# Optimization experiments

Measured on AMD Instinct MI355X. Metric: run time of the kernel, lower is better.

## Reference

```python
import jax, jax.numpy as jnp
import numpy as np

OBS_DIM, ACT_DIM, H_DIM = 128, 32, 512
B, T, N = 32, 64, 64


def setup_inputs() -> dict:
    key = jax.random.key(0)
    ks = jax.random.split(key, 8)
    in_dim = OBS_DIM + ACT_DIM
    s_ih = 1.0 / np.sqrt(H_DIM)
    return {
        "obs_hist": jax.random.normal(ks[0], (B, T, N, OBS_DIM), jnp.float32),
        "action_hist": jax.random.normal(ks[1], (B, T, N, ACT_DIM), jnp.float32),
        "w_ih": jax.random.uniform(ks[2], (3 * H_DIM, in_dim), jnp.float32, -s_ih, s_ih),
        "w_hh": jax.random.uniform(ks[3], (3 * H_DIM, H_DIM), jnp.float32, -s_ih, s_ih),
        "b_ih": jax.random.uniform(ks[4], (3 * H_DIM,), jnp.float32, -s_ih, s_ih),
        "b_hh": jax.random.uniform(ks[5], (3 * H_DIM,), jnp.float32, -s_ih, s_ih),
        "w_dec": jax.random.uniform(ks[6], (OBS_DIM, H_DIM), jnp.float32, -s_ih, s_ih),
        "b_dec": jax.random.uniform(ks[7], (OBS_DIM,), jnp.float32, -s_ih, s_ih),
        "horizon": 63,
    }


def _gru_cell(x, h, w_ih, w_hh, b_ih, b_hh):
    # torch.nn.GRUCell gate order: r, z, n
    gi = x @ w_ih.T + b_ih          # (bn, 3h)
    gh = h @ w_hh.T + b_hh          # (bn, 3h)
    i_r, i_z, i_n = jnp.split(gi, 3, axis=-1)
    h_r, h_z, h_n = jnp.split(gh, 3, axis=-1)
    r = jax.nn.sigmoid(i_r + h_r)
    z = jax.nn.sigmoid(i_z + h_z)
    n = jnp.tanh(i_n + r * h_n)
    return (1.0 - z) * n + z * h


def reference(obs_hist, action_hist, w_ih, w_hh, b_ih, b_hh, w_dec, b_dec, horizon):
    b, t, n, d = obs_hist.shape
    hd = w_hh.shape[1]
    # teacher forcing with horizon <= t-1: step s consumes obs_hist[:, s]
    # time-leading inputs for scan: (horizon, b*n, d+a)
    xs = jnp.concatenate([obs_hist[:, :horizon], action_hist[:, :horizon]], axis=-1)
    xs = xs.transpose(1, 0, 2, 3).reshape(horizon, b * n, -1)
    h0 = jnp.zeros((b * n, hd), obs_hist.dtype)

    def step(h, inp):
        h = _gru_cell(inp, h, w_ih, w_hh, b_ih, b_hh)
        pred = h @ w_dec.T + b_dec  # (bn, d)
        return h, (pred, h)

    _, (preds, hs) = jax.lax.scan(step, h0, xs)
    preds = preds.reshape(horizon, b, n, d).transpose(1, 0, 2, 3)  # (b, horizon, n, d)
    hs = hs.reshape(horizon, b, n, hd).transpose(1, 0, 2, 3)       # (b, horizon, n, h)
    return preds, hs
```

## Files before the change

kernel.cpp:

```cpp
#include <hip/hip_runtime.h>
#include <stdint.h>

typedef _Float16 half_t;
typedef _Float16 half8 __attribute__((ext_vector_type(8)));
typedef _Float16 half4 __attribute__((ext_vector_type(4)));
typedef float f32x16 __attribute__((ext_vector_type(16)));
typedef float f32x4  __attribute__((ext_vector_type(4)));

#define OBS_D 128
#define ACT_D 32
#define IN_D  160
#define H_D   512
#define T_H   63
#define NROWS 2048
#define KTOT  672
#define KT_ALL 42
#define KT_X   10
#define KT_H   32
#define NT_ALL 48
#define NBLK   64
#define NG     16
#define NC     16
#define NFLAG_WORDS (NG*T_H*NC)
#define PRED_ELEMS (NROWS*T_H*OBS_D)

#define ZERO16 {0.f,0.f,0.f,0.f,0.f,0.f,0.f,0.f,0.f,0.f,0.f,0.f,0.f,0.f,0.f,0.f}
#define MFMA16 __builtin_amdgcn_mfma_f32_32x32x16_f16

__device__ __forceinline__ float sigm(float x) {
    return __builtin_amdgcn_rcpf(1.0f + __expf(-x));
}
__device__ __forceinline__ float tanh_f(float x) {
    return 2.0f * __builtin_amdgcn_rcpf(1.0f + __expf(-2.0f * x)) - 1.0f;
}

__global__ void pack_w(const float* __restrict__ w_ih, const float* __restrict__ w_hh,
                       const float* __restrict__ w_dec,
                       half_t* __restrict__ wpack, half_t* __restrict__ wdpack) {
    int idx = blockIdx.x * 256 + threadIdx.x;
    int lane = idx & 63;
    int m = lane & 31;
    int khalf = lane >> 5;
    if (idx < NT_ALL * KT_ALL * 64) {
        int kt = (idx >> 6) % KT_ALL;
        int nt = idx / (64 * KT_ALL);
        int n = nt * 32 + m;
        int k0 = kt * 16 + khalf * 8;
        half8 o;
        #pragma unroll
        for (int j = 0; j < 8; ++j) {
            int k = k0 + j;
            float v = (k < IN_D) ? w_ih[(size_t)n * IN_D + k]
                                 : w_hh[(size_t)n * H_D + (k - IN_D)];
            o[j] = (half_t)v;
        }
        *(half8*)(wpack + (size_t)idx * 8) = o;
    } else {
        int r = idx - NT_ALL * KT_ALL * 64;
        int kt = (r >> 6) % 32;
        int nt = r / (64 * 32);
        int n = nt * 32 + m;
        int k0 = kt * 16 + khalf * 8;
        half8 o;
        #pragma unroll
        for (int j = 0; j < 8; ++j) o[j] = (half_t)w_dec[(size_t)n * H_D + k0 + j];
        *(half8*)(wdpack + (size_t)r * 8) = o;
    }
}

__global__ void pack_x(const float* __restrict__ obs, const float* __restrict__ act,
                       half_t* __restrict__ xfrag, unsigned* __restrict__ flags) {
    int idx = blockIdx.x * 256 + threadIdx.x;
    if (idx < NFLAG_WORDS)
        __hip_atomic_store(&flags[idx], 0u, __ATOMIC_RELAXED, __HIP_MEMORY_SCOPE_AGENT);
    int lane = idx & 63;
    int kt = (idx >> 6) % KT_X;
    int t  = (idx / (64 * KT_X)) % T_H;
    int rb = idx / (64 * KT_X * T_H);
    int m = lane & 31;
    int row = rb * 32 + m;
    int b = row >> 6, nn = row & 63;
    int k0 = kt * 16 + (lane >> 5) * 8;
    const float* ob = obs + (((size_t)(b * 64 + t)) * 64 + nn) * OBS_D;
    const float* ac = act + (((size_t)(b * 64 + t)) * 64 + nn) * ACT_D;
    half8 o;
    #pragma unroll
    for (int j = 0; j < 8; ++j) {
        int k = k0 + j;
        float v = (k < OBS_D) ? ob[k] : ac[k - OBS_D];
        o[j] = (half_t)v;
    }
    *(half8*)(xfrag + (size_t)idx * 8) = o;
}

__global__ __launch_bounds__(256, 1) void gru_main(
        const half_t* __restrict__ wpack, const half_t* __restrict__ xfrag,
        const float* __restrict__ b_ih, const float* __restrict__ b_hh,
        float* __restrict__ out, unsigned* __restrict__ flags) {
    __shared__ __align__(16) half_t Bl[3 * KT_ALL * 512];

    const int tid = threadIdx.x;
    const int wv = tid >> 6;
    const int lane = tid & 63;
    const int col = lane & 31;
    const int khalf = lane >> 5;
    const int mbase = khalf * 4;
    const int g  = blockIdx.x & 15;
    const int cb = blockIdx.x >> 4;

    {
        uint4* dst = (uint4*)Bl;
        #pragma unroll
        for (int gi = 0; gi < 3; ++gi) {
            const uint4* src = (const uint4*)(wpack +
                ((size_t)(gi * 16 + cb) * KT_ALL) * 512);
            for (int s = tid; s < KT_ALL * 64; s += 256)
                dst[gi * (KT_ALL * 64) + s] = src[s];
        }
    }

    const int d = cb * 32 + col;
    const float br = b_ih[d] + b_hh[d];
    const float bz = b_ih[512 + d] + b_hh[512 + d];
    const float bi = b_ih[1024 + d];
    const float bh = b_hh[1024 + d];

    const int bq  = g * 2 + (wv >> 1);
    const int nnq = (wv & 1) * 32;
    const int rrow = lane & 31;

    const half_t* xb = xfrag + ((size_t)(g * 4 + wv) * T_H) * (KT_X * 512) + lane * 8;

    float* hsw = out + (size_t)PRED_ELEMS
               + ((size_t)bq * T_H) * (64 * 512) + (size_t)nnq * 512;

    float h[16];
    #pragma unroll
    for (int i = 0; i < 16; ++i) h[i] = 0.0f;

    const half8* Br = (const half8*)Bl;
    const half8* Bz = (const half8*)(Bl + 21504);
    const half8* Bn = (const half8*)(Bl + 43008);

    __syncthreads();

    for (int t = 0; ; ++t) {
        f32x16 ar, az, ai, ah;
        #pragma unroll
        for (int i = 0; i < 16; ++i) { ar[i] = br; az[i] = bz; ai[i] = bi; ah[i] = bh; }

        {
            const half_t* xt = xb + (size_t)t * (KT_X * 512);
            #pragma unroll
            for (int kt = 0; kt < KT_X; ++kt) {
                half8 a = *(const half8*)(xt + kt * 512);
                ar = MFMA16(a, Br[kt * 64 + lane], ar, 0, 0, 0);
                az = MFMA16(a, Bz[kt * 64 + lane], az, 0, 0, 0);
                ai = MFMA16(a, Bn[kt * 64 + lane], ai, 0, 0, 0);
            }
        }
        if (t > 0) {
            const float* hp = hsw + (size_t)(t - 1) * (64 * 512)
                            + (size_t)rrow * 512 + khalf * 8;
            #pragma unroll 8
            for (int kt = KT_X; kt < KT_ALL; ++kt) {
                int hd = (kt - KT_X) * 16;
                f32x4 v0 = *(const f32x4*)(hp + hd);
                f32x4 v1 = *(const f32x4*)(hp + hd + 4);
                half8 a;
                a[0] = (half_t)v0[0]; a[1] = (half_t)v0[1];
                a[2] = (half_t)v0[2]; a[3] = (half_t)v0[3];
                a[4] = (half_t)v1[0]; a[5] = (half_t)v1[1];
                a[6] = (half_t)v1[2]; a[7] = (half_t)v1[3];
                ar = MFMA16(a, Br[kt * 64 + lane], ar, 0, 0, 0);
                az = MFMA16(a, Bz[kt * 64 + lane], az, 0, 0, 0);
                ah = MFMA16(a, Bn[kt * 64 + lane], ah, 0, 0, 0);
            }
        }

        {
            float* hw = hsw + (size_t)t * (64 * 512);
            #pragma unroll
            for (int r = 0; r < 16; ++r) {
                int m = (r & 3) + 8 * (r >> 2) + mbase;
                float rr = sigm(ar[r]);
                float zz2 = sigm(az[r]);
                float nn2 = tanh_f(ai[r] + rr * ah[r]);
                float hv = (1.0f - zz2) * nn2 + zz2 * h[r];
                h[r] = hv;
                __hip_atomic_store(hw + (size_t)m * 512 + d, hv,
                                   __ATOMIC_RELAXED, __HIP_MEMORY_SCOPE_AGENT);
            }
        }

        if (t == T_H - 1) break;

        __syncthreads();

        unsigned* fb = flags + (size_t)(g * T_H + t) * NC;
        if (tid == 0)
            __hip_atomic_store(fb + cb, 1u,
                               __ATOMIC_RELEASE, __HIP_MEMORY_SCOPE_AGENT);
        if (tid < NC) {
            int guard = 0;
            while (__hip_atomic_load(fb + tid, __ATOMIC_ACQUIRE,
                                     __HIP_MEMORY_SCOPE_AGENT) == 0u) {
                if (++guard > (1 << 15)) break;
            }
        }
        __syncthreads();
    }
}

#define DPAD 520
__global__ __launch_bounds__(256) void dec_k(
        const float* __restrict__ hs, const half_t* __restrict__ wdpack,
        const float* __restrict__ b_dec, float* __restrict__ preds) {
    __shared__ __align__(16) half_t Ab[32 * DPAD];
    const int tid = threadIdx.x, w = tid >> 6, lane = tid & 63;
    const size_t row0 = (size_t)blockIdx.x * 32;

    const float* src = hs + row0 * 512;
    #pragma unroll
    for (int c = 0; c < 16; ++c) {
        int f = c * 1024 + tid * 4;
        f32x4 v = *(const f32x4*)(src + f);
        int m = f >> 9, colc = f & 511;
        half4 o;
        o[0] = (half_t)v[0]; o[1] = (half_t)v[1]; o[2] = (half_t)v[2]; o[3] = (half_t)v[3];
        *(half4*)(Ab + m * DPAD + colc) = o;
    }
    __syncthreads();

    f32x16 acc = ZERO16;
    const half_t* wd = wdpack + ((size_t)w * 32) * 512 + lane * 8;
    const int mA = lane & 31, k0 = (lane >> 5) * 8;
    #pragma unroll 4
    for (int kt = 0; kt < 32; ++kt) {
        half8 a = *(const half8*)(Ab + mA * DPAD + kt * 16 + k0);
        half8 b = *(const half8*)(wd + kt * 512);
        acc = MFMA16(a, b, acc, 0, 0, 0);
    }
    const int colD = w * 32 + (lane & 31);
    const float bd = b_dec[colD];
    #pragma unroll
    for (int r = 0; r < 16; ++r) {
        int m = (r & 3) + 8 * (r >> 2) + 4 * (lane >> 5);
        preds[(row0 + m) * 128 + colD] = acc[r] + bd;
    }
}

extern "C" void kernel_launch(void* const* d_in, const int* in_sizes, int n_in,
                              void* d_out, int out_size, void* d_ws, size_t ws_size,
                              hipStream_t stream) {
    const float* obs   = (const float*)d_in[0];
    const float* act   = (const float*)d_in[1];
    const float* w_ih  = (const float*)d_in[2];
    const float* w_hh  = (const float*)d_in[3];
    const float* b_ih  = (const float*)d_in[4];
    const float* b_hh  = (const float*)d_in[5];
    const float* w_dec = (const float*)d_in[6];
    const float* b_dec = (const float*)d_in[7];
    float* out = (float*)d_out;

    half_t* wpack  = (half_t*)d_ws;
    half_t* wdpack = wpack + (size_t)NT_ALL * KT_ALL * 512;
    half_t* xfrag  = wdpack + (size_t)4 * 32 * 512;
    unsigned* flags = (unsigned*)(xfrag + (size_t)NBLK * T_H * (KT_X * 512));

    hipLaunchKernelGGL(pack_w, dim3(536), dim3(256), 0, stream,
                       w_ih, w_hh, w_dec, wpack, wdpack);
    hipLaunchKernelGGL(pack_x, dim3(10080), dim3(256), 0, stream,
                       obs, act, xfrag, flags);
    hipLaunchKernelGGL(gru_main, dim3(NG * NC), dim3(256), 0, stream,
                       wpack, xfrag, b_ih, b_hh, out, flags);
    hipLaunchKernelGGL(dec_k, dim3(NROWS * T_H / 32), dim3(256), 0, stream,
                       out + (size_t)PRED_ELEMS, wdpack, b_dec, out);
}
```

Baseline: 1.505 ms.

## Overlap next-step input projection with grid barrier wait and prefetch h loads

Computes the x-part MFMA accumulation for step t+1 between signalling the flag and spinning on the cross-block barrier, so input-projection work hides the synchronisation latency. It also software-pipelines the fp32 h-state loads in the recurrent part, issuing the next 8 loads ahead of the MFMAs. The flag store and load are relaxed from release/acquire to relaxed, which removes fences but risks other blocks reading stale h values. The spin guard limit is doubled.

```diff
diff --git a/kernel.cpp b/kernel.cpp
--- a/kernel.cpp
+++ b/kernel.cpp
@@ -142,39 +142,56 @@
     const half8* Bz = (const half8*)(Bl + 21504);
     const half8* Bn = (const half8*)(Bl + 43008);
 
+    f32x16 ar, az, ai, ah;
+
+#define ACC_INIT() do { _Pragma("unroll") \
+    for (int i_ = 0; i_ < 16; ++i_) { ar[i_]=br; az[i_]=bz; ai[i_]=bi; ah[i_]=bh; } \
+    } while (0)
+
+#define XPART(TT) do { const half_t* xt_ = xb + (size_t)(TT) * (KT_X * 512); \
+    _Pragma("unroll") \
+    for (int kt_ = 0; kt_ < KT_X; ++kt_) { \
+        half8 a_ = *(const half8*)(xt_ + kt_ * 512); \
+        ar = MFMA16(a_, Br[kt_ * 64 + lane], ar, 0, 0, 0); \
+        az = MFMA16(a_, Bz[kt_ * 64 + lane], az, 0, 0, 0); \
+        ai = MFMA16(a_, Bn[kt_ * 64 + lane], ai, 0, 0, 0); \
+    } } while (0)
+
     __syncthreads();
 
+    ACC_INIT();
+    XPART(0);
+
     for (int t = 0; ; ++t) {
-        f32x16 ar, az, ai, ah;
-        #pragma unroll
-        for (int i = 0; i < 16; ++i) { ar[i] = br; az[i] = bz; ai[i] = bi; ah[i] = bh; }
-
-        {
-            const half_t* xt = xb + (size_t)t * (KT_X * 512);
-            #pragma unroll
-            for (int kt = 0; kt < KT_X; ++kt) {
-                half8 a = *(const half8*)(xt + kt * 512);
-                ar = MFMA16(a, Br[kt * 64 + lane], ar, 0, 0, 0);
-                az = MFMA16(a, Bz[kt * 64 + lane], az, 0, 0, 0);
-                ai = MFMA16(a, Bn[kt * 64 + lane], ai, 0, 0, 0);
-            }
-        }
         if (t > 0) {
             const float* hp = hsw + (size_t)(t - 1) * (64 * 512)
                             + (size_t)rrow * 512 + khalf * 8;
-            #pragma unroll 8
-            for (int kt = KT_X; kt < KT_ALL; ++kt) {
-                int hd = (kt - KT_X) * 16;
-                f32x4 v0 = *(const f32x4*)(hp + hd);
-                f32x4 v1 = *(const f32x4*)(hp + hd + 4);
-                half8 a;
-                a[0] = (half_t)v0[0]; a[1] = (half_t)v0[1];
-                a[2] = (half_t)v0[2]; a[3] = (half_t)v0[3];
-                a[4] = (half_t)v1[0]; a[5] = (half_t)v1[1];
-                a[6] = (half_t)v1[2]; a[7] = (half_t)v1[3];
-                ar = MFMA16(a, Br[kt * 64 + lane], ar, 0, 0, 0);
-                az = MFMA16(a, Bz[kt * 64 + lane], az, 0, 0, 0);
-                ah = MFMA16(a, Bn[kt * 64 + lane], ah, 0, 0, 0);
+            f32x4 va[8], vb[8];
+            #pragma unroll
+            for (int i = 0; i < 8; ++i) {
+                va[i] = *(const f32x4*)(hp + i * 16);
+                vb[i] = *(const f32x4*)(hp + i * 16 + 4);
+            }
+            #pragma unroll
+            for (int blk = 0; blk < 4; ++blk) {
+                #pragma unroll
+                for (int i = 0; i < 8; ++i) {
+                    const int kt = blk * 8 + i;
+                    f32x4 nva, nvb;
+                    if (blk < 3) {
+                        nva = *(const f32x4*)(hp + (kt + 8) * 16);
+                        nvb = *(const f32x4*)(hp + (kt + 8) * 16 + 4);
+                    }
+                    half8 a;
+                    a[0]=(half_t)va[i][0]; a[1]=(half_t)va[i][1];
+                    a[2]=(half_t)va[i][2]; a[3]=(half_t)va[i][3];
+                    a[4]=(half_t)vb[i][0]; a[5]=(half_t)vb[i][1];
+                    a[6]=(half_t)vb[i][2]; a[7]=(half_t)vb[i][3];
+                    ar = MFMA16(a, Br[(KT_X + kt) * 64 + lane], ar, 0, 0, 0);
+                    az = MFMA16(a, Bz[(KT_X + kt) * 64 + lane], az, 0, 0, 0);
+                    ah = MFMA16(a, Bn[(KT_X + kt) * 64 + lane], ah, 0, 0, 0);
+                    if (blk < 3) { va[i] = nva; vb[i] = nvb; }
+                }
             }
         }
 
@@ -200,16 +217,22 @@
         unsigned* fb = flags + (size_t)(g * T_H + t) * NC;
         if (tid == 0)
             __hip_atomic_store(fb + cb, 1u,
-                               __ATOMIC_RELEASE, __HIP_MEMORY_SCOPE_AGENT);
+                               __ATOMIC_RELAXED, __HIP_MEMORY_SCOPE_AGENT);
+
+        ACC_INIT();
+        XPART(t + 1);
+
         if (tid < NC) {
             int guard = 0;
-            while (__hip_atomic_load(fb + tid, __ATOMIC_ACQUIRE,
+            while (__hip_atomic_load(fb + tid, __ATOMIC_RELAXED,
                                      __HIP_MEMORY_SCOPE_AGENT) == 0u) {
-                if (++guard > (1 << 15)) break;
+                if (++guard > (1 << 16)) break;
             }
         }
         __syncthreads();
     }
+#undef ACC_INIT
+#undef XPART
 }
 
 #define DPAD 520
```

Result: faster. 1.262 ms (-16.1%).
